# Kernel optimization log

Hardware: AMD Instinct MI355X
Metric: run time of the kernel (lower is better)

Reference implementation:

```python
import jax, jax.numpy as jnp
import numpy as np

B, N, D = 8, 2048, 1024
NEG = -1e9


def setup_inputs() -> dict:
    key = jax.random.key(0)
    kx, kl, kq, kk, kv, ko = jax.random.split(key, 6)
    x = jax.random.normal(kx, (B, N, D), dtype=jnp.float32)
    # prefix padding mask: each clip has a random valid length in [N//2, N]
    lengths = jax.random.randint(kl, (B,), N // 2, N + 1)
    mask = jnp.arange(N)[None, :] < lengths[:, None]  # [B, N] bool
    s = 1.0 / np.sqrt(D)
    Wq = jax.random.normal(kq, (D, D), dtype=jnp.float32) * s  # nn.Linear weight [out,in]
    Wk = jax.random.normal(kk, (D, D), dtype=jnp.float32) * s
    Wv = jax.random.normal(kv, (D, D), dtype=jnp.float32) * s
    Wo = jax.random.normal(ko, (D, D), dtype=jnp.float32) * s
    return {"x": x, "mask": mask, "Wq": Wq, "Wk": Wk, "Wv": Wv, "Wo": Wo}


def reference(x, mask, Wq, Wk, Wv, Wo):
    # Linear (no bias): y = x @ W.T
    K = jnp.einsum('bnd,ed->bne', x, Wk)
    Q = jnp.einsum('bnd,ed->bne', x, Wq) * 0.06
    V = jnp.einsum('bnd,ed->bne', x, Wv)
    logits = jnp.einsum('bne,bme->bnm', Q, K)  # [B, N, N]
    # attention_mask = outer product of padding mask (matmul of mask with its transpose)
    attn_mask = mask[:, :, None] & mask[:, None, :]
    logits = jnp.where(attn_mask, logits, NEG)
    att_weights = jax.nn.softmax(logits, axis=-1)
    # dropout (p=0.5) is identity in eval mode
    # y = (V^T @ W)^T  ->  y[b,i,:] = sum_j att[b,j,i] * V[b,j,:]
    y = jnp.einsum('bji,bjd->bid', att_weights, V)
    y = jnp.einsum('bid,ed->bie', y, Wo)
    return (y, att_weights)
```

## Files before the change

### kernel.cpp

```cpp
#include <hip/hip_runtime.h>
#include <math.h>

typedef __attribute__((ext_vector_type(8))) short short8;
typedef __attribute__((ext_vector_type(4))) float f32x4;

namespace {
constexpr int B_ = 8;
constexpr int N_ = 2048;
constexpr int D_ = 1024;
constexpr float NEGV = -1.0e9f;
}

__device__ __forceinline__ unsigned short f2bf(float x) {
    union { float f; unsigned u; } v; v.f = x;
    unsigned u = v.u + 0x7fffu + ((v.u >> 16) & 1u);
    return (unsigned short)(u >> 16);
}

__global__ __launch_bounds__(256)
void k_lengths(const unsigned char* __restrict__ mask, int* __restrict__ L)
{
    const int b = blockIdx.x;
    const int t = threadIdx.x;
    const bool u8 = (mask[1] != 0);
    int cnt = 0;
    if (u8) {
        for (int n = t; n < N_; n += 256)
            cnt += (mask[(size_t)b * N_ + n] != 0) ? 1 : 0;
    } else {
        const int* mi = (const int*)mask;
        for (int n = t; n < N_; n += 256)
            cnt += (mi[(size_t)b * N_ + n] != 0) ? 1 : 0;
    }
    __shared__ int red[256];
    red[t] = cnt;
    __syncthreads();
    for (int s = 128; s > 0; s >>= 1) {
        if (t < s) red[t] += red[t + s];
        __syncthreads();
    }
    if (t == 0) L[b] = red[0];
}

__global__ __launch_bounds__(256)
void convert_bf16(const float* __restrict__ in, unsigned short* __restrict__ out,
                  int n4, float alpha)
{
    const int i = blockIdx.x * 256 + threadIdx.x;
    if (i >= n4) return;
    const float4 v = ((const float4*)in)[i];
    ushort4 o;
    o.x = f2bf(v.x * alpha); o.y = f2bf(v.y * alpha);
    o.z = f2bf(v.z * alpha); o.w = f2bf(v.w * alpha);
    ((ushort4*)out)[i] = o;
}

template <int OUT_MODE>
__global__ __launch_bounds__(256)
void gemm_nt_mfma(const unsigned short* __restrict__ A, int lda, long strideA,
                  const unsigned short* __restrict__ Bm, int ldb, long strideB,
                  void* __restrict__ Cout, int ldc, long strideC,
                  int K, const int* __restrict__ Lp)
{
    __shared__ __attribute__((aligned(16))) short As[128 * 32];
    __shared__ __attribute__((aligned(16))) short Bs[128 * 32];

    const int tid  = threadIdx.x;
    const int lane = tid & 63;
    const int wave = tid >> 6;

    const unsigned gx   = gridDim.x;
    const unsigned gxy  = gx * gridDim.y;
    const unsigned total = gxy * gridDim.z;
    const unsigned orig = blockIdx.x + gx * blockIdx.y + gxy * blockIdx.z;
    unsigned wg = orig;
    if ((total & 7u) == 0u)
        wg = (orig & 7u) * (total >> 3) + (orig >> 3);
    const unsigned bz  = wg / gxy;
    const unsigned rem = wg - bz * gxy;
    const unsigned byy = rem / gx;
    const unsigned bxx = rem - byy * gx;

    const int b    = (int)bz;
    const int m0   = (int)byy * 128;
    const int n0   = (int)bxx * 128;

    const unsigned short* Ab = A  + (long)b * strideA;
    const unsigned short* Bb = Bm + (long)b * strideB;

    const int rowL = tid >> 2;
    const int rowH = (tid + 256) >> 2;
    const int seg  = (((tid & 3) ^ ((tid >> 3) & 3)) * 8);

    const unsigned short* gA0 = Ab + (long)(m0 + rowL) * lda + seg;
    const unsigned short* gA1 = Ab + (long)(m0 + rowH) * lda + seg;
    const unsigned short* gB0 = Bb + (long)(n0 + rowL) * ldb + seg;
    const unsigned short* gB1 = Bb + (long)(n0 + rowH) * ldb + seg;

    short* lA0 = As + ((tid & ~63) + 0)   * 8;
    short* lA1 = As + ((tid & ~63) + 256) * 8;
    short* lB0 = Bs + ((tid & ~63) + 0)   * 8;
    short* lB1 = Bs + ((tid & ~63) + 256) * 8;

    const int q = lane >> 4, r = lane & 15;
    const int wm = (wave & 1) * 64, wn = (wave >> 1) * 64;
    const int sphys = (q ^ ((r >> 1) & 3)) * 8;

    const short* pa[4];
    const short* pb[4];
#pragma unroll
    for (int t = 0; t < 4; ++t) {
        pa[t] = As + (wm + t * 16 + r) * 32 + sphys;
        pb[t] = Bs + (wn + t * 16 + r) * 32 + sphys;
    }

    f32x4 acc[4][4] = {};

    for (int k0 = 0; k0 < K; k0 += 32) {
        __syncthreads();
        __builtin_amdgcn_global_load_lds(
            (const __attribute__((address_space(1))) void*)(gA0 + k0),
            (__attribute__((address_space(3))) void*)lA0, 16, 0, 0);
        __builtin_amdgcn_global_load_lds(
            (const __attribute__((address_space(1))) void*)(gB0 + k0),
            (__attribute__((address_space(3))) void*)lB0, 16, 0, 0);
        __builtin_amdgcn_global_load_lds(
            (const __attribute__((address_space(1))) void*)(gA1 + k0),
            (__attribute__((address_space(3))) void*)lA1, 16, 0, 0);
        __builtin_amdgcn_global_load_lds(
            (const __attribute__((address_space(1))) void*)(gB1 + k0),
            (__attribute__((address_space(3))) void*)lB1, 16, 0, 0);
        __syncthreads();

        short8 af[4], bf[4];
#pragma unroll
        for (int t = 0; t < 4; ++t) {
            af[t] = *(const short8*)pa[t];
            bf[t] = *(const short8*)pb[t];
        }
#pragma unroll
        for (int mt = 0; mt < 4; ++mt)
#pragma unroll
            for (int nt = 0; nt < 4; ++nt)
                acc[mt][nt] = __builtin_amdgcn_mfma_f32_16x16x32_bf16(
                    af[mt], bf[nt], acc[mt][nt], 0, 0, 0);
    }

    if (OUT_MODE == 1) {
        unsigned short* C = (unsigned short*)Cout + (long)b * strideC;
#pragma unroll
        for (int mt = 0; mt < 4; ++mt)
#pragma unroll
            for (int nt = 0; nt < 4; ++nt)
#pragma unroll
                for (int rr = 0; rr < 4; ++rr) {
                    const int grow = m0 + wm + mt * 16 + q * 4 + rr;
                    const int gcol = n0 + wn + nt * 16 + r;
                    C[(long)grow * ldc + gcol] = f2bf(acc[mt][nt][rr]);
                }
    } else if (OUT_MODE == 0) {
        float* C = (float*)Cout + (long)b * strideC;
#pragma unroll
        for (int mt = 0; mt < 4; ++mt)
#pragma unroll
            for (int nt = 0; nt < 4; ++nt)
#pragma unroll
                for (int rr = 0; rr < 4; ++rr) {
                    const int grow = m0 + wm + mt * 16 + q * 4 + rr;
                    const int gcol = n0 + wn + nt * 16 + r;
                    C[(long)grow * ldc + gcol] = acc[mt][nt][rr];
                }
    } else {
        const int Lb = Lp[b];
        float* C = (float*)Cout + (long)b * strideC;
#pragma unroll
        for (int mt = 0; mt < 4; ++mt)
#pragma unroll
            for (int nt = 0; nt < 4; ++nt)
#pragma unroll
                for (int rr = 0; rr < 4; ++rr) {
                    const int grow = m0 + wm + mt * 16 + q * 4 + rr;
                    const int gcol = n0 + wn + nt * 16 + r;
                    const float val = (grow < Lb && gcol < Lb) ? acc[mt][nt][rr] : NEGV;
                    C[(long)grow * ldc + gcol] = val;
                }
    }
}

__global__ __launch_bounds__(256)
void softmax_rows(float* __restrict__ Att)
{
    const size_t row = blockIdx.x;
    float* p = Att + row * (size_t)N_;
    const int t = threadIdx.x;

    float4 v0 = *(float4*)(p + t * 4);
    float4 v1 = *(float4*)(p + 1024 + t * 4);

    float mx = fmaxf(fmaxf(fmaxf(v0.x, v0.y), fmaxf(v0.z, v0.w)),
                     fmaxf(fmaxf(v1.x, v1.y), fmaxf(v1.z, v1.w)));
#pragma unroll
    for (int o = 32; o > 0; o >>= 1) mx = fmaxf(mx, __shfl_xor(mx, o, 64));

    __shared__ float red[8];
    const int wv = t >> 6;
    if ((t & 63) == 0) red[wv] = mx;
    __syncthreads();
    mx = fmaxf(fmaxf(red[0], red[1]), fmaxf(red[2], red[3]));

    float e[8];
    e[0] = expf(v0.x - mx); e[1] = expf(v0.y - mx);
    e[2] = expf(v0.z - mx); e[3] = expf(v0.w - mx);
    e[4] = expf(v1.x - mx); e[5] = expf(v1.y - mx);
    e[6] = expf(v1.z - mx); e[7] = expf(v1.w - mx);
    float s = ((e[0] + e[1]) + (e[2] + e[3])) + ((e[4] + e[5]) + (e[6] + e[7]));
#pragma unroll
    for (int o = 32; o > 0; o >>= 1) s += __shfl_xor(s, o, 64);
    if ((t & 63) == 0) red[4 + wv] = s;
    __syncthreads();
    const float inv = 1.0f / (red[4] + red[5] + red[6] + red[7]);

    *(float4*)(p + t * 4)        = make_float4(e[0] * inv, e[1] * inv, e[2] * inv, e[3] * inv);
    *(float4*)(p + 1024 + t * 4) = make_float4(e[4] * inv, e[5] * inv, e[6] * inv, e[7] * inv);
}

__global__ __launch_bounds__(256)
void transpose_att_bf16(const float* __restrict__ att, unsigned short* __restrict__ attT)
{
    __shared__ float tile[64][65];
    const int b  = blockIdx.z;
    const int j0 = blockIdx.y * 64;
    const int i0 = blockIdx.x * 64;
    const float* src = att + (long)b * N_ * N_;
    unsigned short* dst = attT + (long)b * N_ * N_;
    const int t = threadIdx.x;
#pragma unroll
    for (int l = 0; l < 4; ++l) {
        const int idx = t + l * 256;
        const int jj = idx >> 4;
        const int i4 = (idx & 15) * 4;
        const float4 v = *(const float4*)(src + (long)(j0 + jj) * N_ + i0 + i4);
        tile[i4 + 0][jj] = v.x;
        tile[i4 + 1][jj] = v.y;
        tile[i4 + 2][jj] = v.z;
        tile[i4 + 3][jj] = v.w;
    }
    __syncthreads();
#pragma unroll
    for (int l = 0; l < 4; ++l) {
        const int idx = t + l * 256;
        const int ii = idx >> 4;
        const int j4 = (idx & 15) * 4;
        ushort4 o;
        o.x = f2bf(tile[ii][j4 + 0]);
        o.y = f2bf(tile[ii][j4 + 1]);
        o.z = f2bf(tile[ii][j4 + 2]);
        o.w = f2bf(tile[ii][j4 + 3]);
        *(ushort4*)(dst + (long)(i0 + ii) * N_ + j0 + j4) = o;
    }
}

__global__ __launch_bounds__(256)
void transpose_v_bf16(const unsigned short* __restrict__ qkv, unsigned short* __restrict__ vt)
{
    __shared__ unsigned short tile[64][68];
    const int j0 = blockIdx.x * 64;
    const int d0 = blockIdx.y * 64;
    const int t = threadIdx.x;
#pragma unroll
    for (int l = 0; l < 4; ++l) {
        const int idx = t + l * 256;
        const int jj = idx >> 4;
        const int d4 = (idx & 15) * 4;
        const ushort4 v = *(const ushort4*)(qkv + (long)(j0 + jj) * 3072 + 2048 + d0 + d4);
        tile[d4 + 0][jj] = v.x;
        tile[d4 + 1][jj] = v.y;
        tile[d4 + 2][jj] = v.z;
        tile[d4 + 3][jj] = v.w;
    }
    __syncthreads();
#pragma unroll
    for (int l = 0; l < 4; ++l) {
        const int idx = t + l * 256;
        const int dd = idx >> 4;
        const int j4 = (idx & 15) * 4;
        ushort4 o;
        o.x = tile[dd][j4 + 0];
        o.y = tile[dd][j4 + 1];
        o.z = tile[dd][j4 + 2];
        o.w = tile[dd][j4 + 3];
        *(ushort4*)(vt + (long)(d0 + dd) * 16384 + j0 + j4) = o;
    }
}

extern "C" void kernel_launch(void* const* d_in, const int* in_sizes, int n_in,
                              void* d_out, int out_size, void* d_ws, size_t ws_size,
                              hipStream_t stream)
{
    const float* x  = (const float*)d_in[0];
    const unsigned char* mask = (const unsigned char*)d_in[1];
    const float* Wq = (const float*)d_in[2];
    const float* Wk = (const float*)d_in[3];
    const float* Wv = (const float*)d_in[4];
    const float* Wo = (const float*)d_in[5];

    float* y   = (float*)d_out;
    float* att = (float*)d_out + (size_t)B_ * N_ * D_;

    char* ws = (char*)d_ws;
    int* L = (int*)ws;
    unsigned short* Wqkvb = (unsigned short*)(ws + 256);
    unsigned short* Wob   = Wqkvb + 3145728;
    unsigned short* xb    = Wob + 1048576;
    unsigned short* QKVb  = xb + 16777216;
    unsigned short* VT    = QKVb + 50331648;
    unsigned short* attT  = QKVb;
    unsigned short* ctx   = xb;

    const dim3 blk(256);
    const long NN = (long)N_ * N_;
    const long ND = (long)N_ * D_;
    const long NQ = (long)N_ * 3072;

    k_lengths<<<dim3(B_), blk, 0, stream>>>(mask, L);

    convert_bf16<<<dim3(16384), blk, 0, stream>>>(x,  xb,  4194304, 1.0f);
    convert_bf16<<<dim3(1024),  blk, 0, stream>>>(Wq, Wqkvb,           262144, 0.06f);
    convert_bf16<<<dim3(1024),  blk, 0, stream>>>(Wk, Wqkvb + 1048576, 262144, 1.0f);
    convert_bf16<<<dim3(1024),  blk, 0, stream>>>(Wv, Wqkvb + 2097152, 262144, 1.0f);
    convert_bf16<<<dim3(1024),  blk, 0, stream>>>(Wo, Wob,             262144, 1.0f);

    gemm_nt_mfma<1><<<dim3(24, 128, 1), blk, 0, stream>>>(
        xb, D_, 0, Wqkvb, D_, 0, QKVb, 3072, 0, D_, nullptr);

    transpose_v_bf16<<<dim3(256, 16), blk, 0, stream>>>(QKVb, VT);

    gemm_nt_mfma<2><<<dim3(16, 16, B_), blk, 0, stream>>>(
        QKVb, 3072, NQ, QKVb + 1024, 3072, NQ, att, N_, NN, D_, L);

    softmax_rows<<<dim3(B_ * N_), blk, 0, stream>>>(att);

    transpose_att_bf16<<<dim3(32, 32, B_), blk, 0, stream>>>(att, attT);

    gemm_nt_mfma<1><<<dim3(8, 16, B_), blk, 0, stream>>>(
        attT, N_, NN, VT, B_ * N_, N_, ctx, D_, ND, N_, nullptr);

    gemm_nt_mfma<0><<<dim3(8, 128, 1), blk, 0, stream>>>(
        ctx, D_, 0, Wob, D_, 0, y, D_, 0, D_, nullptr);
}
```

Baseline: 730.5 us.

## Replace GEMM with 256x256 double-buffered pipelined MFMA kernel and masked-tile skip

```diff
diff --git a/kernel.cpp b/kernel.cpp
--- a/kernel.cpp
+++ b/kernel.cpp
@@ -55,22 +55,25 @@
     ((ushort4*)out)[i] = o;
 }
 
-template <int OUT_MODE>
-__global__ __launch_bounds__(256)
-void gemm_nt_mfma(const unsigned short* __restrict__ A, int lda, long strideA,
-                  const unsigned short* __restrict__ Bm, int ldb, long strideB,
-                  void* __restrict__ Cout, int ldc, long strideC,
-                  int K, const int* __restrict__ Lp)
-{
-    __shared__ __attribute__((aligned(16))) short As[128 * 32];
-    __shared__ __attribute__((aligned(16))) short Bs[128 * 32];
+template <int OUT_MODE, bool MFAST>
+__global__ __launch_bounds__(512, 2)
+void gemm_nt_256(const unsigned short* __restrict__ A, int lda, long strideA,
+                 const unsigned short* __restrict__ Bm, int ldb, long strideB,
+                 void* __restrict__ Cout, int ldc, long strideC,
+                 int K, const int* __restrict__ Lp)
+{
+    __shared__ __attribute__((aligned(16))) short As[2][16384];
+    __shared__ __attribute__((aligned(16))) short Bs[2][16384];
 
     const int tid  = threadIdx.x;
     const int lane = tid & 63;
     const int wave = tid >> 6;
+    const int wr   = wave >> 2;
+    const int wc   = wave & 3;
 
     const unsigned gx   = gridDim.x;
-    const unsigned gxy  = gx * gridDim.y;
+    const unsigned gy   = gridDim.y;
+    const unsigned gxy  = gx * gy;
     const unsigned total = gxy * gridDim.z;
     const unsigned orig = blockIdx.x + gx * blockIdx.y + gxy * blockIdx.z;
     unsigned wg = orig;
@@ -78,109 +81,181 @@
         wg = (orig & 7u) * (total >> 3) + (orig >> 3);
     const unsigned bz  = wg / gxy;
     const unsigned rem = wg - bz * gxy;
-    const unsigned byy = rem / gx;
-    const unsigned bxx = rem - byy * gx;
-
-    const int b    = (int)bz;
-    const int m0   = (int)byy * 128;
-    const int n0   = (int)bxx * 128;
+    unsigned byy, bxx;
+    if (MFAST) { byy = rem % gy; bxx = rem / gy; }
+    else       { byy = rem / gx; bxx = rem % gx; }
+
+    const int b  = (int)bz;
+    const int m0 = (int)byy * 256;
+    const int n0 = (int)bxx * 256;
+
+    int Lb = 0;
+    if (OUT_MODE == 2) {
+        Lb = Lp[b];
+        if (m0 >= Lb || n0 >= Lb) {
+            float* C = (float*)Cout + (long)b * strideC;
+            const float4 nv = make_float4(NEGV, NEGV, NEGV, NEGV);
+            const int rl = tid >> 6;
+            const int c4 = (tid & 63) * 4;
+#pragma unroll
+            for (int l = 0; l < 32; ++l)
+                *(float4*)(C + (long)(m0 + l * 8 + rl) * ldc + n0 + c4) = nv;
+            return;
+        }
+    }
 
     const unsigned short* Ab = A  + (long)b * strideA;
     const unsigned short* Bb = Bm + (long)b * strideB;
 
-    const int rowL = tid >> 2;
-    const int rowH = (tid + 256) >> 2;
-    const int seg  = (((tid & 3) ^ ((tid >> 3) & 3)) * 8);
-
-    const unsigned short* gA0 = Ab + (long)(m0 + rowL) * lda + seg;
-    const unsigned short* gA1 = Ab + (long)(m0 + rowH) * lda + seg;
-    const unsigned short* gB0 = Bb + (long)(n0 + rowL) * ldb + seg;
-    const unsigned short* gB1 = Bb + (long)(n0 + rowH) * ldb + seg;
-
-    short* lA0 = As + ((tid & ~63) + 0)   * 8;
-    short* lA1 = As + ((tid & ~63) + 256) * 8;
-    short* lB0 = Bs + ((tid & ~63) + 0)   * 8;
-    short* lB1 = Bs + ((tid & ~63) + 256) * 8;
-
-    const int q = lane >> 4, r = lane & 15;
-    const int wm = (wave & 1) * 64, wn = (wave >> 1) * 64;
-    const int sphys = (q ^ ((r >> 1) & 3)) * 8;
-
-    const short* pa[4];
-    const short* pb[4];
-#pragma unroll
-    for (int t = 0; t < 4; ++t) {
-        pa[t] = As + (wm + t * 16 + r) * 32 + sphys;
-        pb[t] = Bs + (wn + t * 16 + r) * 32 + sphys;
-    }
-
-    f32x4 acc[4][4] = {};
-
-    for (int k0 = 0; k0 < K; k0 += 32) {
-        __syncthreads();
-        __builtin_amdgcn_global_load_lds(
-            (const __attribute__((address_space(1))) void*)(gA0 + k0),
-            (__attribute__((address_space(3))) void*)lA0, 16, 0, 0);
-        __builtin_amdgcn_global_load_lds(
-            (const __attribute__((address_space(1))) void*)(gB0 + k0),
-            (__attribute__((address_space(3))) void*)lB0, 16, 0, 0);
-        __builtin_amdgcn_global_load_lds(
-            (const __attribute__((address_space(1))) void*)(gA1 + k0),
-            (__attribute__((address_space(3))) void*)lA1, 16, 0, 0);
-        __builtin_amdgcn_global_load_lds(
-            (const __attribute__((address_space(1))) void*)(gB1 + k0),
-            (__attribute__((address_space(3))) void*)lB1, 16, 0, 0);
-        __syncthreads();
-
-        short8 af[4], bf[4];
-#pragma unroll
-        for (int t = 0; t < 4; ++t) {
-            af[t] = *(const short8*)pa[t];
-            bf[t] = *(const short8*)pb[t];
-        }
-#pragma unroll
-        for (int mt = 0; mt < 4; ++mt)
-#pragma unroll
-            for (int nt = 0; nt < 4; ++nt)
-                acc[mt][nt] = __builtin_amdgcn_mfma_f32_16x16x32_bf16(
-                    af[mt], bf[nt], acc[mt][nt], 0, 0, 0);
-    }
-
+    const int srow = tid >> 3;
+    const int sseg = ((tid & 7) ^ ((tid >> 4) & 7)) * 8;
+    const unsigned short* gA = Ab + (long)(m0 + srow) * lda + sseg;
+    const unsigned short* gB = Bb + (long)(n0 + srow) * ldb + sseg;
+    const int ldst = (tid & ~63) * 8;
+
+    const int q  = lane >> 4, r = lane & 15;
+    const int h8 = (r >> 1) & 7;
+    const int arb = (wr * 128 + r) * 64;
+    const int brb = (wc * 64 + r) * 64;
+    int pk[2];
+    pk[0] = (q ^ h8) * 8;
+    pk[1] = pk[0] ^ 32;
+
+    const int NT = K >> 6;
+
+    short8 aF[8][2];
+    short8 bF[4][2];
+    f32x4  acc[8][4] = {};
+
+#define STAGE_A2(dd, hh, kt) do {                                              \
+    __builtin_amdgcn_global_load_lds(                                          \
+        (const __attribute__((address_space(1))) void*)(gA + (long)((hh)*128)*lda + (long)(kt)*64),      \
+        (__attribute__((address_space(3))) void*)(&As[dd][(hh)*8192 + ldst]), 16, 0, 0);                 \
+    __builtin_amdgcn_global_load_lds(                                          \
+        (const __attribute__((address_space(1))) void*)(gA + (long)((hh)*128 + 64)*lda + (long)(kt)*64), \
+        (__attribute__((address_space(3))) void*)(&As[dd][(hh)*8192 + 4096 + ldst]), 16, 0, 0);          \
+} while (0)
+
+#define STAGE_B2(dd, hh, kt) do {                                              \
+    __builtin_amdgcn_global_load_lds(                                          \
+        (const __attribute__((address_space(1))) void*)(gB + (long)((hh)*128)*ldb + (long)(kt)*64),      \
+        (__attribute__((address_space(3))) void*)(&Bs[dd][(hh)*8192 + ldst]), 16, 0, 0);                 \
+    __builtin_amdgcn_global_load_lds(                                          \
+        (const __attribute__((address_space(1))) void*)(gB + (long)((hh)*128 + 64)*ldb + (long)(kt)*64), \
+        (__attribute__((address_space(3))) void*)(&Bs[dd][(hh)*8192 + 4096 + ldst]), 16, 0, 0);          \
+} while (0)
+
+#define LDA_F(dd, mrep, ks) aF[mrep][ks] = *(const short8*)&As[dd][arb + (mrep)*1024 + pk[ks]]
+#define LDB_F(dd, nrep, ks) bF[nrep][ks] = *(const short8*)&Bs[dd][brb + (nrep)*1024 + pk[ks]]
+
+#define BARX __builtin_amdgcn_s_barrier()
+#define WAIT_LGKM0 do { asm volatile("s_waitcnt lgkmcnt(0)" ::: "memory"); \
+                        __builtin_amdgcn_sched_barrier(0); } while (0)
+#define WAIT_VM0   do { asm volatile("s_waitcnt vmcnt(0)"   ::: "memory"); \
+                        __builtin_amdgcn_sched_barrier(0); } while (0)
+#define WAIT_VM2   do { asm volatile("s_waitcnt vmcnt(2)"   ::: "memory"); \
+                        __builtin_amdgcn_sched_barrier(0); } while (0)
+#define WAIT_VM4   do { asm volatile("s_waitcnt vmcnt(4)"   ::: "memory"); \
+                        __builtin_amdgcn_sched_barrier(0); } while (0)
+
+#define MFMA_Q(mh, nh) do {                                                    \
+    __builtin_amdgcn_s_setprio(1);                                             \
+    _Pragma("unroll") for (int mr = 0; mr < 4; ++mr)                           \
+    _Pragma("unroll") for (int nr = 0; nr < 2; ++nr)                           \
+    _Pragma("unroll") for (int ks = 0; ks < 2; ++ks)                           \
+        acc[(mh)*4+mr][(nh)*2+nr] = __builtin_amdgcn_mfma_f32_16x16x32_bf16(   \
+            aF[(mh)*4+mr][ks], bF[(nh)*2+nr][ks], acc[(mh)*4+mr][(nh)*2+nr], 0, 0, 0); \
+    __builtin_amdgcn_s_setprio(0);                                             \
+} while (0)
+
+#define TILE_STEP(d, kt) do {                                                  \
+                                                                       \
+    LDB_F(d, 2, 0); LDB_F(d, 2, 1); LDB_F(d, 3, 0); LDB_F(d, 3, 1);            \
+    LDA_F(d, 4, 0); LDA_F(d, 4, 1); LDA_F(d, 5, 0); LDA_F(d, 5, 1);            \
+    if ((kt) + 1 < NT) STAGE_B2((d) ^ 1, 0, (kt) + 1);                         \
+    BARX; WAIT_LGKM0; MFMA_Q(0, 0); BARX;                                      \
+                                                                       \
+    LDA_F(d, 6, 0); LDA_F(d, 6, 1); LDA_F(d, 7, 0); LDA_F(d, 7, 1);            \
+    if ((kt) + 1 < NT) STAGE_B2((d) ^ 1, 1, (kt) + 1);                         \
+    BARX; WAIT_LGKM0; MFMA_Q(0, 1); BARX;                                      \
+          \
+    if ((kt) + 2 < NT) { STAGE_A2(d, 0, (kt) + 2); WAIT_VM2; }                 \
+    else               { WAIT_VM0; }                                           \
+    BARX; WAIT_LGKM0; MFMA_Q(1, 0); BARX;                                      \
+                                                                       \
+    if ((kt) + 1 < NT) {                                                       \
+        LDA_F((d) ^ 1, 0, 0); LDA_F((d) ^ 1, 0, 1);                            \
+        LDA_F((d) ^ 1, 1, 0); LDA_F((d) ^ 1, 1, 1);                            \
+        LDA_F((d) ^ 1, 2, 0); LDA_F((d) ^ 1, 2, 1);                            \
+        LDA_F((d) ^ 1, 3, 0); LDA_F((d) ^ 1, 3, 1);                            \
+        LDB_F((d) ^ 1, 0, 0); LDB_F((d) ^ 1, 0, 1);                            \
+        LDB_F((d) ^ 1, 1, 0); LDB_F((d) ^ 1, 1, 1);                            \
+    }                                                                          \
+    if ((kt) + 2 < NT) STAGE_A2(d, 1, (kt) + 2);                               \
+    BARX; WAIT_LGKM0; MFMA_Q(1, 1); BARX;                                      \
+} while (0)
+
+    STAGE_A2(0, 0, 0); STAGE_A2(0, 1, 0);
+    STAGE_B2(0, 0, 0); STAGE_B2(0, 1, 0);
+    STAGE_A2(1, 0, 1); STAGE_A2(1, 1, 1);
+    WAIT_VM4; BARX;
+    LDA_F(0, 0, 0); LDA_F(0, 0, 1); LDA_F(0, 1, 0); LDA_F(0, 1, 1);
+    LDA_F(0, 2, 0); LDA_F(0, 2, 1); LDA_F(0, 3, 0); LDA_F(0, 3, 1);
+    LDB_F(0, 0, 0); LDB_F(0, 0, 1); LDB_F(0, 1, 0); LDB_F(0, 1, 1);
+
+    for (int kt = 0; kt < NT; kt += 2) {
+        TILE_STEP(0, kt);
+        TILE_STEP(1, kt + 1);
+    }
+
+#undef STAGE_A2
+#undef STAGE_B2
+#undef LDA_F
+#undef LDB_F
+#undef BARX
+#undef WAIT_LGKM0
+#undef WAIT_VM0
+#undef WAIT_VM2
+#undef WAIT_VM4
+#undef MFMA_Q
+#undef TILE_STEP
+
+    const int rbase = m0 + wr * 128;
+    const int cbase = n0 + wc * 64;
     if (OUT_MODE == 1) {
         unsigned short* C = (unsigned short*)Cout + (long)b * strideC;
 #pragma unroll
-        for (int mt = 0; mt < 4; ++mt)
+        for (int mt = 0; mt < 8; ++mt)
 #pragma unroll
             for (int nt = 0; nt < 4; ++nt)
 #pragma unroll
                 for (int rr = 0; rr < 4; ++rr) {
-                    const int grow = m0 + wm + mt * 16 + q * 4 + rr;
-                    const int gcol = n0 + wn + nt * 16 + r;
+                    const int grow = rbase + mt * 16 + q * 4 + rr;
+                    const int gcol = cbase + nt * 16 + r;
                     C[(long)grow * ldc + gcol] = f2bf(acc[mt][nt][rr]);
                 }
     } else if (OUT_MODE == 0) {
         float* C = (float*)Cout + (long)b * strideC;
 #pragma unroll
-        for (int mt = 0; mt < 4; ++mt)
+        for (int mt = 0; mt < 8; ++mt)
 #pragma unroll
             for (int nt = 0; nt < 4; ++nt)
 #pragma unroll
                 for (int rr = 0; rr < 4; ++rr) {
-                    const int grow = m0 + wm + mt * 16 + q * 4 + rr;
-                    const int gcol = n0 + wn + nt * 16 + r;
+                    const int grow = rbase + mt * 16 + q * 4 + rr;
+                    const int gcol = cbase + nt * 16 + r;
                     C[(long)grow * ldc + gcol] = acc[mt][nt][rr];
                 }
     } else {
-        const int Lb = Lp[b];
         float* C = (float*)Cout + (long)b * strideC;
 #pragma unroll
-        for (int mt = 0; mt < 4; ++mt)
+        for (int mt = 0; mt < 8; ++mt)
 #pragma unroll
             for (int nt = 0; nt < 4; ++nt)
 #pragma unroll
                 for (int rr = 0; rr < 4; ++rr) {
-                    const int grow = m0 + wm + mt * 16 + q * 4 + rr;
-                    const int gcol = n0 + wn + nt * 16 + r;
+                    const int grow = rbase + mt * 16 + q * 4 + rr;
+                    const int gcol = cbase + nt * 16 + r;
                     const float val = (grow < Lb && gcol < Lb) ? acc[mt][nt][rr] : NEGV;
                     C[(long)grow * ldc + gcol] = val;
                 }
@@ -318,6 +393,7 @@
     unsigned short* ctx   = xb;
 
     const dim3 blk(256);
+    const dim3 blk512(512);
     const long NN = (long)N_ * N_;
     const long ND = (long)N_ * D_;
     const long NQ = (long)N_ * 3072;
@@ -330,21 +406,21 @@
     convert_bf16<<<dim3(1024),  blk, 0, stream>>>(Wv, Wqkvb + 2097152, 262144, 1.0f);
     convert_bf16<<<dim3(1024),  blk, 0, stream>>>(Wo, Wob,             262144, 1.0f);
 
-    gemm_nt_mfma<1><<<dim3(24, 128, 1), blk, 0, stream>>>(
+    gemm_nt_256<1, true><<<dim3(12, 64, 1), blk512, 0, stream>>>(
         xb, D_, 0, Wqkvb, D_, 0, QKVb, 3072, 0, D_, nullptr);
 
     transpose_v_bf16<<<dim3(256, 16), blk, 0, stream>>>(QKVb, VT);
 
-    gemm_nt_mfma<2><<<dim3(16, 16, B_), blk, 0, stream>>>(
+    gemm_nt_256<2, false><<<dim3(8, 8, B_), blk512, 0, stream>>>(
         QKVb, 3072, NQ, QKVb + 1024, 3072, NQ, att, N_, NN, D_, L);
 
     softmax_rows<<<dim3(B_ * N_), blk, 0, stream>>>(att);
 
     transpose_att_bf16<<<dim3(32, 32, B_), blk, 0, stream>>>(att, attT);
 
-    gemm_nt_mfma<1><<<dim3(8, 16, B_), blk, 0, stream>>>(
+    gemm_nt_256<1, true><<<dim3(4, 8, B_), blk512, 0, stream>>>(
         attT, N_, NN, VT, B_ * N_, N_, ctx, D_, ND, N_, nullptr);
 
-    gemm_nt_mfma<0><<<dim3(8, 128, 1), blk, 0, stream>>>(
+    gemm_nt_256<0, false><<<dim3(4, 64, 1), blk512, 0, stream>>>(
         ctx, D_, 0, Wob, D_, 0, y, D_, 0, D_, nullptr);
 }
```

Result: slower. 811.7 us (+11.1%).

## Double-buffer GEMM LDS tiles and skip padded tiles and rows in attention

Applied to the files above, without the earlier changes.

```diff
diff --git a/kernel.cpp b/kernel.cpp
--- a/kernel.cpp
+++ b/kernel.cpp
@@ -56,14 +56,14 @@
 }
 
 template <int OUT_MODE>
-__global__ __launch_bounds__(256)
-void gemm_nt_mfma(const unsigned short* __restrict__ A, int lda, long strideA,
-                  const unsigned short* __restrict__ Bm, int ldb, long strideB,
-                  void* __restrict__ Cout, int ldc, long strideC,
-                  int K, const int* __restrict__ Lp)
-{
-    __shared__ __attribute__((aligned(16))) short As[128 * 32];
-    __shared__ __attribute__((aligned(16))) short Bs[128 * 32];
+__global__ __launch_bounds__(256, 3)
+void gemm_nt_128(const unsigned short* __restrict__ A, int lda, long strideA,
+                 const unsigned short* __restrict__ Bm, int ldb, long strideB,
+                 void* __restrict__ Cout, int ldc, long strideC,
+                 int K, const int* __restrict__ Lp)
+{
+    __shared__ __attribute__((aligned(16))) short As[2][128 * 32];
+    __shared__ __attribute__((aligned(16))) short Bs[2][128 * 32];
 
     const int tid  = threadIdx.x;
     const int lane = tid & 63;
@@ -81,9 +81,25 @@
     const unsigned byy = rem / gx;
     const unsigned bxx = rem - byy * gx;
 
-    const int b    = (int)bz;
-    const int m0   = (int)byy * 128;
-    const int n0   = (int)bxx * 128;
+    const int b  = (int)bz;
+    const int m0 = (int)byy * 128;
+    const int n0 = (int)bxx * 128;
+
+    int Lb = 0;
+    if (OUT_MODE == 2) {
+        Lb = Lp[b];
+        if (m0 >= Lb) return;
+        if (n0 >= Lb) {
+            float* C = (float*)Cout + (long)b * strideC;
+            const float4 nv = make_float4(NEGV, NEGV, NEGV, NEGV);
+            const int rl = tid >> 5;
+            const int c4 = (tid & 31) * 4;
+#pragma unroll
+            for (int l = 0; l < 16; ++l)
+                *(float4*)(C + (long)(m0 + l * 8 + rl) * ldc + n0 + c4) = nv;
+            return;
+        }
+    }
 
     const unsigned short* Ab = A  + (long)b * strideA;
     const unsigned short* Bb = Bm + (long)b * strideB;
@@ -97,46 +113,51 @@
     const unsigned short* gB0 = Bb + (long)(n0 + rowL) * ldb + seg;
     const unsigned short* gB1 = Bb + (long)(n0 + rowH) * ldb + seg;
 
-    short* lA0 = As + ((tid & ~63) + 0)   * 8;
-    short* lA1 = As + ((tid & ~63) + 256) * 8;
-    short* lB0 = Bs + ((tid & ~63) + 0)   * 8;
-    short* lB1 = Bs + ((tid & ~63) + 256) * 8;
+    const int lA0o = (tid & ~63) * 8;
+    const int lA1o = lA0o + 2048;
 
     const int q = lane >> 4, r = lane & 15;
     const int wm = (wave & 1) * 64, wn = (wave >> 1) * 64;
     const int sphys = (q ^ ((r >> 1) & 3)) * 8;
 
-    const short* pa[4];
-    const short* pb[4];
+    int pao[4], pbo[4];
 #pragma unroll
     for (int t = 0; t < 4; ++t) {
-        pa[t] = As + (wm + t * 16 + r) * 32 + sphys;
-        pb[t] = Bs + (wn + t * 16 + r) * 32 + sphys;
-    }
+        pao[t] = (wm + t * 16 + r) * 32 + sphys;
+        pbo[t] = (wn + t * 16 + r) * 32 + sphys;
+    }
+
+    const int NT = K >> 5;
 
     f32x4 acc[4][4] = {};
 
-    for (int k0 = 0; k0 < K; k0 += 32) {
-        __syncthreads();
-        __builtin_amdgcn_global_load_lds(
-            (const __attribute__((address_space(1))) void*)(gA0 + k0),
-            (__attribute__((address_space(3))) void*)lA0, 16, 0, 0);
-        __builtin_amdgcn_global_load_lds(
-            (const __attribute__((address_space(1))) void*)(gB0 + k0),
-            (__attribute__((address_space(3))) void*)lB0, 16, 0, 0);
-        __builtin_amdgcn_global_load_lds(
-            (const __attribute__((address_space(1))) void*)(gA1 + k0),
-            (__attribute__((address_space(3))) void*)lA1, 16, 0, 0);
-        __builtin_amdgcn_global_load_lds(
-            (const __attribute__((address_space(1))) void*)(gB1 + k0),
-            (__attribute__((address_space(3))) void*)lB1, 16, 0, 0);
-        __syncthreads();
+#define STAGE(dd, kt) do {                                                     \
+    __builtin_amdgcn_global_load_lds(                                          \
+        (const __attribute__((address_space(1))) void*)(gA0 + (long)(kt) * 32),\
+        (__attribute__((address_space(3))) void*)(&As[dd][lA0o]), 16, 0, 0);   \
+    __builtin_amdgcn_global_load_lds(                                          \
+        (const __attribute__((address_space(1))) void*)(gB0 + (long)(kt) * 32),\
+        (__attribute__((address_space(3))) void*)(&Bs[dd][lA0o]), 16, 0, 0);   \
+    __builtin_amdgcn_global_load_lds(                                          \
+        (const __attribute__((address_space(1))) void*)(gA1 + (long)(kt) * 32),\
+        (__attribute__((address_space(3))) void*)(&As[dd][lA1o]), 16, 0, 0);   \
+    __builtin_amdgcn_global_load_lds(                                          \
+        (const __attribute__((address_space(1))) void*)(gB1 + (long)(kt) * 32),\
+        (__attribute__((address_space(3))) void*)(&Bs[dd][lA1o]), 16, 0, 0);   \
+} while (0)
+
+    STAGE(0, 0);
+    __syncthreads();
+
+    for (int kt = 0; kt < NT; ++kt) {
+        const int d = kt & 1;
+        if (kt + 1 < NT) STAGE(d ^ 1, kt + 1);
 
         short8 af[4], bf[4];
 #pragma unroll
         for (int t = 0; t < 4; ++t) {
-            af[t] = *(const short8*)pa[t];
-            bf[t] = *(const short8*)pb[t];
+            af[t] = *(const short8*)&As[d][pao[t]];
+            bf[t] = *(const short8*)&Bs[d][pbo[t]];
         }
 #pragma unroll
         for (int mt = 0; mt < 4; ++mt)
@@ -144,7 +165,11 @@
             for (int nt = 0; nt < 4; ++nt)
                 acc[mt][nt] = __builtin_amdgcn_mfma_f32_16x16x32_bf16(
                     af[mt], bf[nt], acc[mt][nt], 0, 0, 0);
-    }
+
+        __syncthreads();
+    }
+
+#undef STAGE
 
     if (OUT_MODE == 1) {
         unsigned short* C = (unsigned short*)Cout + (long)b * strideC;
@@ -171,7 +196,6 @@
                     C[(long)grow * ldc + gcol] = acc[mt][nt][rr];
                 }
     } else {
-        const int Lb = Lp[b];
         float* C = (float*)Cout + (long)b * strideC;
 #pragma unroll
         for (int mt = 0; mt < 4; ++mt)
@@ -188,11 +212,21 @@
 }
 
 __global__ __launch_bounds__(256)
-void softmax_rows(float* __restrict__ Att)
+void softmax_rows(float* __restrict__ Att, const int* __restrict__ Lp)
 {
     const size_t row = blockIdx.x;
+    const int i = (int)(row & (N_ - 1));
+    const int b = (int)(row >> 11);
     float* p = Att + row * (size_t)N_;
     const int t = threadIdx.x;
+
+    if (i >= Lp[b]) {
+        const float c = 1.0f / 2048.0f;
+        const float4 cv = make_float4(c, c, c, c);
+        *(float4*)(p + t * 4)        = cv;
+        *(float4*)(p + 1024 + t * 4) = cv;
+        return;
+    }
 
     float4 v0 = *(float4*)(p + t * 4);
     float4 v1 = *(float4*)(p + 1024 + t * 4);
@@ -330,21 +364,21 @@
     convert_bf16<<<dim3(1024),  blk, 0, stream>>>(Wv, Wqkvb + 2097152, 262144, 1.0f);
     convert_bf16<<<dim3(1024),  blk, 0, stream>>>(Wo, Wob,             262144, 1.0f);
 
-    gemm_nt_mfma<1><<<dim3(24, 128, 1), blk, 0, stream>>>(
+    gemm_nt_128<1><<<dim3(24, 128, 1), blk, 0, stream>>>(
         xb, D_, 0, Wqkvb, D_, 0, QKVb, 3072, 0, D_, nullptr);
 
     transpose_v_bf16<<<dim3(256, 16), blk, 0, stream>>>(QKVb, VT);
 
-    gemm_nt_mfma<2><<<dim3(16, 16, B_), blk, 0, stream>>>(
+    gemm_nt_128<2><<<dim3(16, 16, B_), blk, 0, stream>>>(
         QKVb, 3072, NQ, QKVb + 1024, 3072, NQ, att, N_, NN, D_, L);
 
-    softmax_rows<<<dim3(B_ * N_), blk, 0, stream>>>(att);
+    softmax_rows<<<dim3(B_ * N_), blk, 0, stream>>>(att, L);
 
     transpose_att_bf16<<<dim3(32, 32, B_), blk, 0, stream>>>(att, attT);
 
-    gemm_nt_mfma<1><<<dim3(8, 16, B_), blk, 0, stream>>>(
+    gemm_nt_128<1><<<dim3(8, 16, B_), blk, 0, stream>>>(
         attT, N_, NN, VT, B_ * N_, N_, ctx, D_, ND, N_, nullptr);
 
-    gemm_nt_mfma<0><<<dim3(8, 128, 1), blk, 0, stream>>>(
+    gemm_nt_128<0><<<dim3(8, 128, 1), blk, 0, stream>>>(
         ctx, D_, 0, Wob, D_, 0, y, D_, 0, D_, nullptr);
 }
```

Measured after the change: 649.4 us. 1.12x faster.
